# Performance work log

Measured on AMD Instinct MI355X. Metric: run time of the kernel, lower is better.

## Reference

```python
import jax, jax.numpy as jnp
import numpy as np

D_MODEL = 1024
NUM_HEADS = 16
THETA = 10000.0
B, S = 4, 2048


def setup_inputs() -> dict:
    key = jax.random.key(0)
    ks = jax.random.split(key, 5)
    scale = 1.0 / np.sqrt(D_MODEL)  # keep logits in a sane range
    return {
        "q_proj_weight": jax.random.normal(ks[0], (D_MODEL, D_MODEL), jnp.float32) * scale,
        "k_proj_weight": jax.random.normal(ks[1], (D_MODEL, D_MODEL), jnp.float32) * scale,
        "v_proj_weight": jax.random.normal(ks[2], (D_MODEL, D_MODEL), jnp.float32) * scale,
        "o_proj_weight": jax.random.normal(ks[3], (D_MODEL, D_MODEL), jnp.float32) * scale,
        "in_features": jax.random.normal(ks[4], (B, S, D_MODEL), jnp.float32),
        "token_positions": jnp.arange(S, dtype=jnp.int32),
    }


def _rope(x, cos, sin):
    # interleaved-pair RoPE: pairs are (x[..., 2i], x[..., 2i+1])
    xe = x[..., 0::2]
    xo = x[..., 1::2]
    re = xe * cos - xo * sin
    ro = xe * sin + xo * cos
    return jnp.stack([re, ro], axis=-1).reshape(x.shape)


def reference(q_proj_weight, k_proj_weight, v_proj_weight, o_proj_weight,
              in_features, token_positions):
    Bv, Sv, _ = in_features.shape
    dk = D_MODEL // NUM_HEADS
    half = dk // 2

    q = in_features @ q_proj_weight.T
    k = in_features @ k_proj_weight.T
    v = in_features @ v_proj_weight.T
    # (B, S, D) -> (B, H, S, dk)
    q = q.reshape(Bv, Sv, NUM_HEADS, dk).transpose(0, 2, 1, 3)
    k = k.reshape(Bv, Sv, NUM_HEADS, dk).transpose(0, 2, 1, 3)
    v = v.reshape(Bv, Sv, NUM_HEADS, dk).transpose(0, 2, 1, 3)

    inv_freq = 1.0 / (THETA ** (jnp.arange(half, dtype=jnp.float32) / half))
    freqs = token_positions.astype(jnp.float32)[:, None] * inv_freq[None, :]  # (S, half)
    cos, sin = jnp.cos(freqs), jnp.sin(freqs)  # broadcast over (B, H, S, half)
    q = _rope(q, cos, sin)
    k = _rope(k, cos, sin)

    scores = jnp.einsum('bhqd,bhkd->bhqk', q, k) / np.sqrt(dk).astype(np.float32)
    causal = jnp.tril(jnp.ones((Sv, Sv), dtype=bool))
    scores = jnp.where(causal, scores, -jnp.inf)
    weights = jax.nn.softmax(scores, axis=-1)
    out = jnp.einsum('bhqk,bhkd->bhqd', weights, v)
    out = out.transpose(0, 2, 1, 3).reshape(Bv, Sv, D_MODEL)
    return out @ o_proj_weight.T
```

## Files before the change

### kernel.cpp

```cpp
#include <hip/hip_runtime.h>
#include <stdint.h>
#include <math.h>

#define NH 16
#define DK 64
#define S_LEN 2048
#define BB 4
#define DM 1024
#define M_TOT (BB*S_LEN)
#define KVT 64
#define KPAD 72
#define QB 128

#define BM 256
#define BN 128
#define BK 64
#define NTK (DM/BK)
#define LDS_A_BUF (BM*BK)
#define LDS_B_BUF (BN*BK)

typedef __attribute__((ext_vector_type(8))) short short8;
typedef __attribute__((ext_vector_type(4))) float floatx4;

typedef const __attribute__((address_space(1))) void gas_t;
typedef __attribute__((address_space(3))) void las_t;

__device__ __forceinline__ void glds16(const void* g, void* l){
  __builtin_amdgcn_global_load_lds((gas_t*)g, (las_t*)l, 16, 0, 0);
}

__device__ __forceinline__ unsigned short f2bf(float f){
  unsigned int u = __float_as_uint(f);
  u += 0x7fffu + ((u >> 16) & 1u);
  return (unsigned short)(u >> 16);
}
__device__ __forceinline__ unsigned int pk_bf_trunc(float a, float b){
  return __builtin_amdgcn_perm(__float_as_uint(b), __float_as_uint(a), 0x07060302u);
}
__device__ __forceinline__ float fast_exp2(float x){
  return __builtin_amdgcn_exp2f(x);
}

__global__ void cast_kernel(const float* __restrict__ in, unsigned short* __restrict__ out, int n){
  int i = (blockIdx.x * blockDim.x + threadIdx.x) * 4;
  if (i < n){
    float4 v = *(const float4*)(in + i);
    ushort4 u;
    u.x = f2bf(v.x); u.y = f2bf(v.y); u.z = f2bf(v.z); u.w = f2bf(v.w);
    *(ushort4*)(out + i) = u;
  }
}

__device__ __forceinline__ void stage_tile(const unsigned short* __restrict__ A,
                                           const unsigned short* __restrict__ Bm,
                                           int m0, int n0, int k0,
                                           unsigned short* As, unsigned short* Bs, int tid)
{
  #pragma unroll
  for (int j = 0; j < 4; j++){
    int c = j*512 + tid;
    int r = c >> 3;
    int sl = (c & 7) ^ (r & 7);
    glds16(&A[(size_t)(m0 + r)*DM + k0 + sl*8], (char*)As + (size_t)c*16);
  }
  #pragma unroll
  for (int j = 0; j < 2; j++){
    int c = j*512 + tid;
    int r = c >> 3;
    int sl = (c & 7) ^ (r & 7);
    glds16(&Bm[(size_t)(n0 + r)*DM + k0 + sl*8], (char*)Bs + (size_t)c*16);
  }
}

__device__ __forceinline__ void gemm_core(const unsigned short* __restrict__ A,
                                          const unsigned short* __restrict__ Bm,
                                          int m0, int n0, unsigned short* Ls,
                                          int tid, floatx4 (&acc)[4][4])
{
  unsigned short* AsB = Ls;
  unsigned short* BsB = Ls + 3*LDS_A_BUF;
  int wave = tid >> 6, lane = tid & 63;
  int l15 = lane & 15, quad = lane >> 4;
  int wm = (wave >> 1) * 64, wn = (wave & 1) * 64;
  int s0 = quad ^ (l15 & 7);

  stage_tile(A, Bm, m0, n0, 0,  AsB,             BsB,             tid);
  stage_tile(A, Bm, m0, n0, BK, AsB + LDS_A_BUF, BsB + LDS_B_BUF, tid);
  asm volatile("s_waitcnt vmcnt(6)" ::: "memory");
  __builtin_amdgcn_s_barrier();

  #pragma unroll
  for (int t = 0; t < NTK; ++t){
    const int bufc = t % 3;
    if (t + 2 < NTK){
      const int bn = (t + 2) % 3;
      stage_tile(A, Bm, m0, n0, (t+2)*BK, AsB + bn*LDS_A_BUF, BsB + bn*LDS_B_BUF, tid);
    }
    const unsigned short* Ab = AsB + bufc*LDS_A_BUF;
    const unsigned short* Bb = BsB + bufc*LDS_B_BUF;
    short8 a[4][2], b[4][2];
    #pragma unroll
    for (int mi = 0; mi < 4; mi++){
      const unsigned short* pr = Ab + (wm + mi*16 + l15)*BK;
      a[mi][0] = *(const short8*)(pr + s0*8);
      a[mi][1] = *(const short8*)(pr + (s0^4)*8);
    }
    #pragma unroll
    for (int ni = 0; ni < 4; ni++){
      const unsigned short* pr = Bb + (wn + ni*16 + l15)*BK;
      b[ni][0] = *(const short8*)(pr + s0*8);
      b[ni][1] = *(const short8*)(pr + (s0^4)*8);
    }
    __builtin_amdgcn_s_setprio(1);
    #pragma unroll
    for (int mi = 0; mi < 4; mi++)
      #pragma unroll
      for (int ni = 0; ni < 4; ni++){
        acc[mi][ni] = __builtin_amdgcn_mfma_f32_16x16x32_bf16(a[mi][0], b[ni][0], acc[mi][ni], 0, 0, 0);
        acc[mi][ni] = __builtin_amdgcn_mfma_f32_16x16x32_bf16(a[mi][1], b[ni][1], acc[mi][ni], 0, 0, 0);
      }
    __builtin_amdgcn_s_setprio(0);
    if (t + 2 < NTK)      { asm volatile("s_waitcnt vmcnt(6)" ::: "memory"); }
    else if (t + 1 < NTK) { asm volatile("s_waitcnt vmcnt(0)" ::: "memory"); }
    if (t + 1 < NTK) __builtin_amdgcn_s_barrier();
  }
}

__global__ __launch_bounds__(512, 2) void gemm_qkv(
    const unsigned short* __restrict__ Xb,
    const unsigned short* __restrict__ Wq,
    const unsigned short* __restrict__ Wk,
    const unsigned short* __restrict__ Wv,
    const int* __restrict__ pos,
    unsigned short* __restrict__ Qo,
    unsigned short* __restrict__ Ko,
    unsigned short* __restrict__ VTo)
{
  __shared__ __align__(16) unsigned short Ls[3*LDS_A_BUF + 3*LDS_B_BUF];
  int m0 = blockIdx.x * BM;
  int n0 = blockIdx.y * BN;
  int z  = blockIdx.z;
  const unsigned short* Bmat = (z == 0) ? Wq : ((z == 1) ? Wk : Wv);
  unsigned short* Out = (z == 0) ? Qo : ((z == 1) ? Ko : VTo);

  int tid = threadIdx.x;
  floatx4 acc[4][4] = {};
  gemm_core(Xb, Bmat, m0, n0, Ls, tid, acc);

  int wave = tid >> 6, lane = tid & 63;
  int l15 = lane & 15, quad = lane >> 4;
  int wm = (wave >> 1) * 64, wn = (wave & 1) * 64;

  if (z == 2){
    #pragma unroll
    for (int mi = 0; mi < 4; mi++){
      int row0 = m0 + wm + mi * 16 + quad * 4;
      int bb2 = row0 >> 11, sQ = row0 & (S_LEN - 1);
      #pragma unroll
      for (int ni = 0; ni < 4; ni++){
        int col = n0 + wn + ni * 16 + l15;
        int h = col >> 6, d = col & 63;
        ushort4 u;
        u.x = f2bf(acc[mi][ni][0]); u.y = f2bf(acc[mi][ni][1]);
        u.z = f2bf(acc[mi][ni][2]); u.w = f2bf(acc[mi][ni][3]);
        *(ushort4*)&Out[(((size_t)bb2 * NH + h) * DK + d) * S_LEN + sQ] = u;
      }
    }
  } else {
    const float SC = (z == 0) ? 0.180336879f : 1.0f;
    #pragma unroll
    for (int mi = 0; mi < 4; mi++){
      #pragma unroll
      for (int ni = 0; ni < 4; ni++){
        int col = n0 + wn + ni * 16 + l15;
        int h = col >> 6, d = col & 63;
        int fi = d >> 1, odd = d & 1;
        float invfrev = fast_exp2(-(float)fi * (13.2877123795494f / 32.0f)) * 0.15915494309f;
        #pragma unroll
        for (int r = 0; r < 4; r++){
          int row = m0 + wm + mi * 16 + quad * 4 + r;
          int bb2 = row >> 11, s = row & (S_LEN - 1);
          float p = (float)pos[s];
          float rev = p * invfrev;
          rev = rev - floorf(rev);
          float c  = __builtin_amdgcn_cosf(rev);
          float sn = __builtin_amdgcn_sinf(rev);
          float val = acc[mi][ni][r];
          float other = __shfl_xor(val, 1);
          float outv = odd ? (other * sn + val * c) : (val * c - other * sn);
          Out[(((size_t)bb2 * NH + h) * S_LEN + s) * DK + d] = f2bf(outv * SC);
        }
      }
    }
  }
}

__global__ __launch_bounds__(512, 2) void gemm_out(
    const unsigned short* __restrict__ Ab,
    const unsigned short* __restrict__ Wo,
    float* __restrict__ Out)
{
  __shared__ __align__(16) unsigned short Ls[3*LDS_A_BUF + 3*LDS_B_BUF];
  int m0 = blockIdx.x * BM;
  int n0 = blockIdx.y * BN;

  int tid = threadIdx.x;
  floatx4 acc[4][4] = {};
  gemm_core(Ab, Wo, m0, n0, Ls, tid, acc);

  int wave = tid >> 6, lane = tid & 63;
  int l15 = lane & 15, quad = lane >> 4;
  int wm = (wave >> 1) * 64, wn = (wave & 1) * 64;

  #pragma unroll
  for (int mi = 0; mi < 4; mi++){
    #pragma unroll
    for (int ni = 0; ni < 4; ni++){
      #pragma unroll
      for (int r = 0; r < 4; r++){
        int row = m0 + wm + mi * 16 + quad * 4 + r;
        int col = n0 + wn + ni * 16 + l15;
        Out[(size_t)row * DM + col] = acc[mi][ni][r];
      }
    }
  }
}

__global__ __launch_bounds__(256) void attn_kernel(
    const unsigned short* __restrict__ Qg,
    const unsigned short* __restrict__ Kg,
    const unsigned short* __restrict__ VTg,
    unsigned short* __restrict__ Ao)
{
  __shared__ __align__(16) unsigned short Ks[KVT * KPAD];
  __shared__ __align__(16) unsigned short Vs[DK * KPAD];
  __shared__ __align__(16) unsigned short Ps[4][32 * KPAD];

  int bh = blockIdx.x;
  int q0 = ((int)gridDim.y - 1 - (int)blockIdx.y) * QB;
  int tid = threadIdx.x, wave = tid >> 6, lane = tid & 63;
  int l15 = lane & 15, quad = lane >> 4;
  int qw = q0 + wave * 32;

  const unsigned short* Qb = Qg + (size_t)bh * S_LEN * DK;
  const unsigned short* Kb = Kg + (size_t)bh * S_LEN * DK;
  const unsigned short* Vb = VTg + (size_t)bh * DK * S_LEN;

  short8 aq[2][2];
  #pragma unroll
  for (int mi = 0; mi < 2; mi++){
    aq[mi][0] = *(const short8*)&Qb[(qw + mi * 16 + l15) * DK + quad * 8];
    aq[mi][1] = *(const short8*)&Qb[(qw + mi * 16 + l15) * DK + 32 + quad * 8];
  }

  floatx4 o[2][4] = {};
  float lsum[2][4] = {{0.f,0.f,0.f,0.f},{0.f,0.f,0.f,0.f}};

  int srow = tid >> 2;
  int scol = (tid & 3) * 16;
  int kpos = (srow & 3) * 16 + (srow >> 2);
  const unsigned short* Krow = Kb + (size_t)srow * DK + scol;
  const unsigned short* Vrow = Vb + (size_t)srow * S_LEN + scol;
  unsigned short* KsW = &Ks[kpos * KPAD + scol];
  unsigned short* VsW = &Vs[srow * KPAD + scol];

  int nt = q0 / KVT + 2;

  short8 kr0 = *(const short8*)(Krow);
  short8 kr1 = *(const short8*)(Krow + 8);
  short8 vr0 = *(const short8*)(Vrow);
  short8 vr1 = *(const short8*)(Vrow + 8);

  for (int kt = 0; kt < nt; kt++){
    int kv0 = kt * KVT;
    __syncthreads();
    *(short8*)(KsW)     = kr0;
    *(short8*)(KsW + 8) = kr1;
    *(short8*)(VsW)     = vr0;
    *(short8*)(VsW + 8) = vr1;
    if (kt + 1 < nt){
      int kvn = kv0 + KVT;
      kr0 = *(const short8*)(Krow + (size_t)kvn * DK);
      kr1 = *(const short8*)(Krow + (size_t)kvn * DK + 8);
      vr0 = *(const short8*)(Vrow + kvn);
      vr1 = *(const short8*)(Vrow + kvn + 8);
    }
    __syncthreads();

    if (kv0 <= qw + 31){
      floatx4 sc[2][4] = {};
      #pragma unroll
      for (int ni = 0; ni < 4; ni++){
        short8 bk0 = *(const short8*)&Ks[(ni * 16 + l15) * KPAD + quad * 8];
        short8 bk1 = *(const short8*)&Ks[(ni * 16 + l15) * KPAD + 32 + quad * 8];
        #pragma unroll
        for (int mi = 0; mi < 2; mi++){
          sc[mi][ni] = __builtin_amdgcn_mfma_f32_16x16x32_bf16(aq[mi][0], bk0, sc[mi][ni], 0, 0, 0);
          sc[mi][ni] = __builtin_amdgcn_mfma_f32_16x16x32_bf16(aq[mi][1], bk1, sc[mi][ni], 0, 0, 0);
        }
      }
      bool full = (kv0 + 63 <= qw);
      int kvb = kv0 + 4 * l15;
      #pragma unroll
      for (int mi = 0; mi < 2; mi++){
        #pragma unroll
        for (int r = 0; r < 4; r++){
          int qg = qw + mi * 16 + quad * 4 + r;
          float v0 = sc[mi][0][r], v1 = sc[mi][1][r], v2 = sc[mi][2][r], v3 = sc[mi][3][r];
          if (!full){
            v0 = (kvb     > qg) ? -INFINITY : v0;
            v1 = (kvb + 1 > qg) ? -INFINITY : v1;
            v2 = (kvb + 2 > qg) ? -INFINITY : v2;
            v3 = (kvb + 3 > qg) ? -INFINITY : v3;
          }
          float p0 = fast_exp2(v0);
          float p1 = fast_exp2(v1);
          float p2 = fast_exp2(v2);
          float p3 = fast_exp2(v3);
          lsum[mi][r] += (p0 + p1) + (p2 + p3);
          uint2 u;
          u.x = pk_bf_trunc(p0, p1);
          u.y = pk_bf_trunc(p2, p3);
          *(uint2*)&Ps[wave][(mi * 16 + quad * 4 + r) * KPAD + 4 * l15] = u;
        }
      }
      asm volatile("s_waitcnt lgkmcnt(0)" ::: "memory");
      short8 ap[2][2];
      #pragma unroll
      for (int mi = 0; mi < 2; mi++){
        ap[mi][0] = *(const short8*)&Ps[wave][(mi * 16 + l15) * KPAD + quad * 8];
        ap[mi][1] = *(const short8*)&Ps[wave][(mi * 16 + l15) * KPAD + 32 + quad * 8];
      }
      #pragma unroll
      for (int dt = 0; dt < 4; dt++){
        short8 bv0 = *(const short8*)&Vs[(dt * 16 + l15) * KPAD + quad * 8];
        short8 bv1 = *(const short8*)&Vs[(dt * 16 + l15) * KPAD + 32 + quad * 8];
        #pragma unroll
        for (int mi = 0; mi < 2; mi++){
          o[mi][dt] = __builtin_amdgcn_mfma_f32_16x16x32_bf16(ap[mi][0], bv0, o[mi][dt], 0, 0, 0);
          o[mi][dt] = __builtin_amdgcn_mfma_f32_16x16x32_bf16(ap[mi][1], bv1, o[mi][dt], 0, 0, 0);
        }
      }
    }
  }

  float linv[2][4];
  #pragma unroll
  for (int mi = 0; mi < 2; mi++){
    #pragma unroll
    for (int r = 0; r < 4; r++){
      float rs = lsum[mi][r];
      rs += __shfl_xor(rs, 1);
      rs += __shfl_xor(rs, 2);
      rs += __shfl_xor(rs, 4);
      rs += __shfl_xor(rs, 8);
      linv[mi][r] = 1.0f / rs;
    }
  }

  int bq = bh >> 4, hq = bh & 15;
  #pragma unroll
  for (int mi = 0; mi < 2; mi++){
    #pragma unroll
    for (int dt = 0; dt < 4; dt++){
      #pragma unroll
      for (int r = 0; r < 4; r++){
        float val = o[mi][dt][r] * linv[mi][r];
        int s = qw + mi * 16 + quad * 4 + r;
        int d = dt * 16 + l15;
        Ao[(((size_t)bq * S_LEN + s) * NH + hq) * DK + d] = f2bf(val);
      }
    }
  }
}

extern "C" void kernel_launch(void* const* d_in, const int* in_sizes, int n_in,
                              void* d_out, int out_size, void* d_ws, size_t ws_size,
                              hipStream_t stream) {
  (void)in_sizes; (void)n_in; (void)out_size; (void)ws_size;
  const float* Wq = (const float*)d_in[0];
  const float* Wk = (const float*)d_in[1];
  const float* Wv = (const float*)d_in[2];
  const float* Wo = (const float*)d_in[3];
  const float* X  = (const float*)d_in[4];
  const int* pos  = (const int*)d_in[5];
  float* out = (float*)d_out;

  char* ws = (char*)d_ws;
  const size_t MB = 1024 * 1024;
  unsigned short* Xb  = (unsigned short*)(ws);
  unsigned short* Wqb = (unsigned short*)(ws + 16 * MB);
  unsigned short* Wkb = (unsigned short*)(ws + 18 * MB);
  unsigned short* Wvb = (unsigned short*)(ws + 20 * MB);
  unsigned short* Wob = (unsigned short*)(ws + 22 * MB);
  unsigned short* Qb  = (unsigned short*)(ws + 24 * MB);
  unsigned short* Kb  = (unsigned short*)(ws + 40 * MB);
  unsigned short* Vb  = (unsigned short*)(ws + 56 * MB);
  unsigned short* Ab  = (unsigned short*)(ws + 72 * MB);

  cast_kernel<<<8192, 256, 0, stream>>>(X,  Xb,  M_TOT * DM);
  cast_kernel<<<1024, 256, 0, stream>>>(Wq, Wqb, DM * DM);
  cast_kernel<<<1024, 256, 0, stream>>>(Wk, Wkb, DM * DM);
  cast_kernel<<<1024, 256, 0, stream>>>(Wv, Wvb, DM * DM);
  cast_kernel<<<1024, 256, 0, stream>>>(Wo, Wob, DM * DM);

  gemm_qkv<<<dim3(M_TOT/BM, DM/BN, 3), 512, 0, stream>>>(Xb, Wqb, Wkb, Wvb, pos, Qb, Kb, Vb);
  attn_kernel<<<dim3(64, S_LEN / QB), 256, 0, stream>>>(Qb, Kb, Vb, Ab);
  gemm_out<<<dim3(M_TOT/BM, DM/BN), 512, 0, stream>>>(Ab, Wob, out);
}
```

Measured before the change: 234.7 us.

## Split GEMM main loop into two phases interleaving staged loads with MFMA

Restructures the bf16 GEMM K-loop into two half-phases. Each phase reads part of the A fragments from LDS, issues half of the next tile's global-to-LDS loads, then runs the matching MFMAs, with extra barriers and lgkmcnt waits between phases. The goal is to interleave global loads, LDS reads and MFMA work across waves, ping-pong style, so memory issue overlaps with matrix math. The cost is several extra workgroup barriers per iteration, which may add sync stalls.

```diff
diff --git a/kernel.cpp b/kernel.cpp
--- a/kernel.cpp
+++ b/kernel.cpp
@@ -29,6 +29,11 @@
   __builtin_amdgcn_global_load_lds((gas_t*)g, (las_t*)l, 16, 0, 0);
 }
 
+#define VMCNT6() asm volatile("s_waitcnt vmcnt(6)" ::: "memory")
+#define VMCNT0() asm volatile("s_waitcnt vmcnt(0)" ::: "memory")
+#define LGKM0()  do{ asm volatile("s_waitcnt lgkmcnt(0)" ::: "memory"); __builtin_amdgcn_sched_barrier(0); }while(0)
+#define BARRIER() asm volatile("s_barrier" ::: "memory")
+
 __device__ __forceinline__ unsigned short f2bf(float f){
   unsigned int u = __float_as_uint(f);
   u += 0x7fffu + ((u >> 16) & 1u);
@@ -51,21 +56,33 @@
   }
 }
 
-__device__ __forceinline__ void stage_tile(const unsigned short* __restrict__ A,
+__device__ __forceinline__ void stage_part(const unsigned short* __restrict__ A,
                                            const unsigned short* __restrict__ Bm,
                                            int m0, int n0, int k0,
-                                           unsigned short* As, unsigned short* Bs, int tid)
+                                           unsigned short* As, unsigned short* Bs,
+                                           int tid, int part)
 {
-  #pragma unroll
-  for (int j = 0; j < 4; j++){
-    int c = j*512 + tid;
+  if (part == 0){
+    #pragma unroll
+    for (int j = 0; j < 2; j++){
+      int c = j*512 + tid;
+      int r = c >> 3;
+      int sl = (c & 7) ^ (r & 7);
+      glds16(&A[(size_t)(m0 + r)*DM + k0 + sl*8], (char*)As + (size_t)c*16);
+    }
+    int c = tid;
     int r = c >> 3;
     int sl = (c & 7) ^ (r & 7);
-    glds16(&A[(size_t)(m0 + r)*DM + k0 + sl*8], (char*)As + (size_t)c*16);
-  }
-  #pragma unroll
-  for (int j = 0; j < 2; j++){
-    int c = j*512 + tid;
+    glds16(&Bm[(size_t)(n0 + r)*DM + k0 + sl*8], (char*)Bs + (size_t)c*16);
+  } else {
+    #pragma unroll
+    for (int j = 2; j < 4; j++){
+      int c = j*512 + tid;
+      int r = c >> 3;
+      int sl = (c & 7) ^ (r & 7);
+      glds16(&A[(size_t)(m0 + r)*DM + k0 + sl*8], (char*)As + (size_t)c*16);
+    }
+    int c = 512 + tid;
     int r = c >> 3;
     int sl = (c & 7) ^ (r & 7);
     glds16(&Bm[(size_t)(n0 + r)*DM + k0 + sl*8], (char*)Bs + (size_t)c*16);
@@ -84,23 +101,26 @@
   int wm = (wave >> 1) * 64, wn = (wave & 1) * 64;
   int s0 = quad ^ (l15 & 7);
 
-  stage_tile(A, Bm, m0, n0, 0,  AsB,             BsB,             tid);
-  stage_tile(A, Bm, m0, n0, BK, AsB + LDS_A_BUF, BsB + LDS_B_BUF, tid);
-  asm volatile("s_waitcnt vmcnt(6)" ::: "memory");
-  __builtin_amdgcn_s_barrier();
+  stage_part(A, Bm, m0, n0, 0,  AsB,             BsB,             tid, 0);
+  stage_part(A, Bm, m0, n0, 0,  AsB,             BsB,             tid, 1);
+  stage_part(A, Bm, m0, n0, BK, AsB + LDS_A_BUF, BsB + LDS_B_BUF, tid, 0);
+  stage_part(A, Bm, m0, n0, BK, AsB + LDS_A_BUF, BsB + LDS_B_BUF, tid, 1);
+  VMCNT6();
+  BARRIER();
 
   #pragma unroll
   for (int t = 0; t < NTK; ++t){
     const int bufc = t % 3;
-    if (t + 2 < NTK){
-      const int bn = (t + 2) % 3;
-      stage_tile(A, Bm, m0, n0, (t+2)*BK, AsB + bn*LDS_A_BUF, BsB + bn*LDS_B_BUF, tid);
-    }
     const unsigned short* Ab = AsB + bufc*LDS_A_BUF;
     const unsigned short* Bb = BsB + bufc*LDS_B_BUF;
-    short8 a[4][2], b[4][2];
-    #pragma unroll
-    for (int mi = 0; mi < 4; mi++){
+    const int bn = (t + 2) % 3;
+    unsigned short* Asn = AsB + bn*LDS_A_BUF;
+    unsigned short* Bsn = BsB + bn*LDS_B_BUF;
+    const int kst = (t + 2) * BK;
+
+    short8 a[2][2], b[4][2];
+    #pragma unroll
+    for (int mi = 0; mi < 2; mi++){
       const unsigned short* pr = Ab + (wm + mi*16 + l15)*BK;
       a[mi][0] = *(const short8*)(pr + s0*8);
       a[mi][1] = *(const short8*)(pr + (s0^4)*8);
@@ -111,18 +131,42 @@
       b[ni][0] = *(const short8*)(pr + s0*8);
       b[ni][1] = *(const short8*)(pr + (s0^4)*8);
     }
+    if (t + 2 < NTK) stage_part(A, Bm, m0, n0, kst, Asn, Bsn, tid, 0);
+    BARRIER();
+    LGKM0();
     __builtin_amdgcn_s_setprio(1);
     #pragma unroll
-    for (int mi = 0; mi < 4; mi++)
+    for (int mi = 0; mi < 2; mi++)
       #pragma unroll
       for (int ni = 0; ni < 4; ni++){
         acc[mi][ni] = __builtin_amdgcn_mfma_f32_16x16x32_bf16(a[mi][0], b[ni][0], acc[mi][ni], 0, 0, 0);
         acc[mi][ni] = __builtin_amdgcn_mfma_f32_16x16x32_bf16(a[mi][1], b[ni][1], acc[mi][ni], 0, 0, 0);
       }
     __builtin_amdgcn_s_setprio(0);
-    if (t + 2 < NTK)      { asm volatile("s_waitcnt vmcnt(6)" ::: "memory"); }
-    else if (t + 1 < NTK) { asm volatile("s_waitcnt vmcnt(0)" ::: "memory"); }
-    if (t + 1 < NTK) __builtin_amdgcn_s_barrier();
+    BARRIER();
+
+    short8 a2[2][2];
+    #pragma unroll
+    for (int mi = 0; mi < 2; mi++){
+      const unsigned short* pr = Ab + (wm + (2 + mi)*16 + l15)*BK;
+      a2[mi][0] = *(const short8*)(pr + s0*8);
+      a2[mi][1] = *(const short8*)(pr + (s0^4)*8);
+    }
+    if (t + 2 < NTK) stage_part(A, Bm, m0, n0, kst, Asn, Bsn, tid, 1);
+    BARRIER();
+    LGKM0();
+    __builtin_amdgcn_s_setprio(1);
+    #pragma unroll
+    for (int mi = 0; mi < 2; mi++)
+      #pragma unroll
+      for (int ni = 0; ni < 4; ni++){
+        acc[2+mi][ni] = __builtin_amdgcn_mfma_f32_16x16x32_bf16(a2[mi][0], b[ni][0], acc[2+mi][ni], 0, 0, 0);
+        acc[2+mi][ni] = __builtin_amdgcn_mfma_f32_16x16x32_bf16(a2[mi][1], b[ni][1], acc[2+mi][ni], 0, 0, 0);
+      }
+    __builtin_amdgcn_s_setprio(0);
+
+    if (t + 2 < NTK)      { VMCNT6(); BARRIER(); }
+    else if (t + 1 < NTK) { VMCNT0(); BARRIER(); }
   }
 }
 
```

Result: slower. 247.5 us (+5.5%).
